# Optimization experiments

Hardware: AMD Instinct MI355X
Metric: run time of the kernel (lower is better)

The kernel has to match this reference:

```python
import jax, jax.numpy as jnp
import numpy as np

B, T, D = 4, 512, 128
HID = 64
INIT = 0.02


def setup_inputs() -> dict:
    key = jax.random.key(0)
    ks = jax.random.split(key, 8)
    h = jax.random.normal(ks[0], (B, T, D), dtype=jnp.float32)
    h_src = jax.random.normal(ks[1], (B, T, D), dtype=jnp.float32)
    # Linear weights stored as (in, out); init std matches cfg.v_phi_init_scale, biases zero.
    W1 = jax.random.normal(ks[2], (3 * D, HID), dtype=jnp.float32) * INIT
    b1 = jnp.zeros((HID,), dtype=jnp.float32)
    W2 = jax.random.normal(ks[3], (HID, HID), dtype=jnp.float32) * INIT
    b2 = jnp.zeros((HID,), dtype=jnp.float32)
    W3 = jax.random.normal(ks[4], (HID, 1), dtype=jnp.float32) * INIT
    b3 = jnp.zeros((1,), dtype=jnp.float32)
    return {"h": h, "h_src": h_src, "W1": W1, "b1": b1, "W2": W2, "b2": b2, "W3": W3, "b3": b3}


def reference(h, h_src, W1, b1, W2, b2, W3, b3):
    # feats = cat(h_q, h_k, h_q - h_k) @ W1  ==  h_q @ (W1q + W1d) + h_k @ (W1k - W1d)
    # This avoids materializing the (B,T,T,3D) concat tensor while computing identical math.
    W1q, W1k, W1d = W1[:D], W1[D:2 * D], W1[2 * D:]
    pq = jnp.einsum('btd,dh->bth', h, W1q + W1d)        # (B,T,HID)
    pk = jnp.einsum('bsd,dh->bsh', h_src, W1k - W1d)    # (B,T,HID)
    x = jax.nn.gelu(pq[:, :, None, :] + pk[:, None, :, :] + b1, approximate=False)  # (B,T,T,HID)
    x = jax.nn.gelu(jnp.einsum('btsh,hk->btsk', x, W2) + b2, approximate=False)
    out = jnp.einsum('btsh,ho->btso', x, W3) + b3       # (B,T,T,1)
    return out[..., 0]                                   # (B,T,T)
```

## Files before the change

kernel.cpp:

```cpp
#include <hip/hip_runtime.h>

#define BB 4
#define TT 512
#define SS 512
#define DD 128
#define HID 64

typedef _Float16 f16;
typedef f16 f16x4 __attribute__((ext_vector_type(4)));
typedef f16 f16x8 __attribute__((ext_vector_type(8)));
typedef float f32x4 __attribute__((ext_vector_type(4)));

#define SPLAT8(c) ((f16x8){(f16)(c),(f16)(c),(f16)(c),(f16)(c),(f16)(c),(f16)(c),(f16)(c),(f16)(c)})

__device__ __forceinline__ f16x8 gelu_pk8(f16x8 x) {
    f16x8 xc = __builtin_elementwise_min(
                   __builtin_elementwise_max(x, SPLAT8(-3.0f)), SPLAT8(3.0f));
    f16x8 xh = xc * SPLAT8(0.5f);
    f16x8 v  = xh * xh;
    f16x8 p  = __builtin_elementwise_fma(v, SPLAT8(-1.96106e-3f), SPLAT8(1.709184e-2f));
    p = __builtin_elementwise_fma(p, v, SPLAT8(-6.617536e-2f));
    p = __builtin_elementwise_fma(p, v, SPLAT8(1.571632e-1f));
    p = __builtin_elementwise_fma(p, v, SPLAT8(-2.665228e-1f));
    p = __builtin_elementwise_fma(p, v, SPLAT8(3.99050e-1f));
    f16x8 t = v * p;
    return __builtin_elementwise_fma(t, SPLAT8(4.0f), x * SPLAT8(0.5f));
}

__global__ __launch_bounds__(256) void pqk_kernel(
    const float* __restrict__ h, const float* __restrict__ h_src,
    const float* __restrict__ W1, const float* __restrict__ b1,
    f16* __restrict__ pq, f16* __restrict__ pk)
{
    const int tid  = threadIdx.x;
    const int wave = tid >> 6;
    const int lane = tid & 63;
    const int g = lane >> 4;
    const int r = lane & 15;

    const int half = blockIdx.x >> 5;
    const int row0 = (blockIdx.x & 31) * 64 + wave * 16;

    const float* src = half ? h_src : h;
    const float* Wa  = W1 + (half ? DD * HID : 0);
    const float* Wd  = W1 + 2 * DD * HID;
    const float  sgn = half ? -1.0f : 1.0f;
    f16* dst = half ? pk : pq;

    f16x8 aw[4][4];
    #pragma unroll
    for (int ks = 0; ks < 4; ++ks) {
        #pragma unroll
        for (int nb = 0; nb < 4; ++nb) {
            const float* wa = Wa + (ks * 32 + g * 8) * HID + nb * 16 + r;
            const float* wd = Wd + (ks * 32 + g * 8) * HID + nb * 16 + r;
            f16x8 v;
            #pragma unroll
            for (int i = 0; i < 8; ++i)
                v[i] = (f16)fmaf(sgn, wd[i * HID], wa[i * HID]);
            aw[ks][nb] = v;
        }
    }

    f16x8 bx[4];
    const float* srow = src + (size_t)(row0 + r) * DD + g * 8;
    #pragma unroll
    for (int ks = 0; ks < 4; ++ks) {
        float4 q0 = *(const float4*)(srow + ks * 32);
        float4 q1 = *(const float4*)(srow + ks * 32 + 4);
        f16x8 v;
        v[0] = (f16)q0.x; v[1] = (f16)q0.y; v[2] = (f16)q0.z; v[3] = (f16)q0.w;
        v[4] = (f16)q1.x; v[5] = (f16)q1.y; v[6] = (f16)q1.z; v[7] = (f16)q1.w;
        bx[ks] = v;
    }

    #pragma unroll
    for (int nb = 0; nb < 4; ++nb) {
        f32x4 acc;
        if (half == 0) {
            float4 bv = *(const float4*)(b1 + nb * 16 + g * 4);
            acc = (f32x4){bv.x, bv.y, bv.z, bv.w};
        } else {
            acc = (f32x4){0.f, 0.f, 0.f, 0.f};
        }
        #pragma unroll
        for (int ks = 0; ks < 4; ++ks)
            acc = __builtin_amdgcn_mfma_f32_16x16x32_f16(aw[ks][nb], bx[ks], acc, 0, 0, 0);
        f16x4 w;
        w[0] = (f16)acc[0]; w[1] = (f16)acc[1];
        w[2] = (f16)acc[2]; w[3] = (f16)acc[3];
        *(f16x4*)(dst + (size_t)(row0 + r) * HID + nb * 16 + g * 4) = w;
    }
}

#define LOADKV(KV0, KV1, CHUNK) {                                         \
    const f16* p_ = pkbase + (size_t)(CHUNK) * 16 * HID;                  \
    (KV0) = *(const f16x8*)(p_);                                          \
    (KV1) = *(const f16x8*)(p_ + 32); }

#define STAGE1(KV0, KV1) {                                                \
    a0 = gelu_pk8(pq0 + (KV0));                                           \
    a1 = gelu_pk8(pq1 + (KV1)); }

#define DOMFMA() {                                                        \
    _Pragma("unroll")                                                     \
    for (int nb = 0; nb < 4; ++nb) {                                      \
        acc[nb] = __builtin_amdgcn_mfma_f32_16x16x32_f16(bw[0][nb], a0, b2i[nb], 0, 0, 0); \
        acc[nb] = __builtin_amdgcn_mfma_f32_16x16x32_f16(bw[1][nb], a1, acc[nb], 0, 0, 0); } }

#define STAGE2(C) {                                                       \
    float tl0 = 0.0f, tl1 = 0.0f, tq0 = 0.0f, tq1 = 0.0f;                 \
    _Pragma("unroll")                                                     \
    for (int nb = 0; nb < 4; ++nb) {                                      \
        _Pragma("unroll")                                                 \
        for (int reg = 0; reg < 4; ++reg) {                               \
            float y = acc[nb][reg];                                       \
            float u = y * y;                                              \
            float cw = (reg == 0) ? w3v[nb].x : (reg == 1) ? w3v[nb].y    \
                     : (reg == 2) ? w3v[nb].z : w3v[nb].w;                \
            if (nb & 1) { tl1 = fmaf(y, cw, tl1); tq1 = fmaf(u, cw, tq1); } \
            else        { tl0 = fmaf(y, cw, tl0); tq0 = fmaf(u, cw, tq0); } \
        }                                                                 \
    }                                                                     \
    float t0 = fmaf(tl0 + tl1, 0.5f, 0.39894228f * (tq0 + tq1));          \
    t0 += __shfl_xor(t0, 16);                                             \
    t0 += __shfl_xor(t0, 32);                                             \
    if (lane < 16) orow[(C) * 16 + lane] = t0 + b3v; }

__global__ __launch_bounds__(256, 4) void main_kernel(
    const f16* __restrict__ pq, const f16* __restrict__ pk,
    const float* __restrict__ W2, const float* __restrict__ b2,
    const float* __restrict__ W3, const float* __restrict__ b3,
    float* __restrict__ out)
{
    const int tid  = threadIdx.x;
    const int wave = tid >> 6;
    const int lane = tid & 63;
    const int g = lane >> 4;
    const int r = lane & 15;

    const int wu  = blockIdx.x * 4 + wave;
    const int bt  = wu >> 2;
    const int sb0 = (wu & 3) * 128;
    const int b   = bt >> 9;

    f16x8 bw[2][4];
    #pragma unroll
    for (int kh = 0; kh < 2; ++kh) {
        #pragma unroll
        for (int nb = 0; nb < 4; ++nb) {
            const float* src = W2 + (kh * 32 + g * 8) * HID + nb * 16 + r;
            f16x8 v;
            #pragma unroll
            for (int i = 0; i < 8; ++i) v[i] = (f16)src[i * HID];
            bw[kh][nb] = v;
        }
    }

    const f16* pqrow = pq + (size_t)bt * HID + g * 8;
    f16x8 pq0 = *(const f16x8*)(pqrow);
    f16x8 pq1 = *(const f16x8*)(pqrow + 32);

    f32x4 b2i[4];
    float4 w3v[4];
    #pragma unroll
    for (int nb = 0; nb < 4; ++nb) {
        float4 bv = *(const float4*)(b2 + nb * 16 + g * 4);
        b2i[nb] = (f32x4){bv.x, bv.y, bv.z, bv.w};
        w3v[nb] = *(const float4*)(W3 + nb * 16 + g * 4);
    }
    const float b3v = b3[0];

    const f16* pkbase = pk + ((size_t)b * SS + sb0 + r) * HID + g * 8;
    float* orow = out + (size_t)bt * SS + sb0;

    f16x8 kvA0, kvA1, kvB0, kvB1;
    f16x8 a0, a1;
    f32x4 acc[4];

    LOADKV(kvA0, kvA1, 0)
    LOADKV(kvB0, kvB1, 1)
    STAGE1(kvA0, kvA1)

    #pragma unroll
    for (int cc = 0; cc < 4; ++cc) {
        DOMFMA()
        if (cc < 3) LOADKV(kvA0, kvA1, 2 * cc + 2)
        STAGE1(kvB0, kvB1)
        STAGE2(2 * cc)

        DOMFMA()
        if (cc < 3) {
            LOADKV(kvB0, kvB1, 2 * cc + 3)
            STAGE1(kvA0, kvA1)
        }
        STAGE2(2 * cc + 1)
    }
}

extern "C" void kernel_launch(void* const* d_in, const int* in_sizes, int n_in,
                              void* d_out, int out_size, void* d_ws, size_t ws_size,
                              hipStream_t stream) {
    const float* h     = (const float*)d_in[0];
    const float* h_src = (const float*)d_in[1];
    const float* W1    = (const float*)d_in[2];
    const float* b1    = (const float*)d_in[3];
    const float* W2    = (const float*)d_in[4];
    const float* b2    = (const float*)d_in[5];
    const float* W3    = (const float*)d_in[6];
    const float* b3    = (const float*)d_in[7];
    float* out = (float*)d_out;

    f16* pq = (f16*)d_ws;
    f16* pk = pq + (size_t)BB * TT * HID;

    pqk_kernel<<<64, 256, 0, stream>>>(h, h_src, W1, b1, pq, pk);
    main_kernel<<<BB * TT * (SS / 128) / 4, 256, 0, stream>>>(pq, pk, W2, b2, W3, b3, out);
}
```

Measured before the change: 36.17 us.

## Fold linear part of second GELU into extra MFMA and absorb b2 algebraically

The second-layer GELU is expanded as a polynomial in the pre-activation. Its linear term, projected through W3, is precomputed as a vector (wlin) plus a constant in an extra block of the first kernel, and the main kernel evaluates it with one additional MFMA pair instead of per-element FMAs. The first GELU is reformulated on the halved input so the 0.5 scaling folds into the pq/pk add and the clamp is removed. This trades a fifth MFMA chain per chunk for fewer VALU ops in the epilogue. The unclamped f16 polynomial and the dropped b2 in the quadratic term may change accuracy, and clvp sits at wlin+HID in f16 units, which is only 4-byte aligned.

Measured after the change: 33.48 us. -7.4%, faster.

```diff
diff --git a/kernel.cpp b/kernel.cpp
--- a/kernel.cpp
+++ b/kernel.cpp
@@ -13,25 +13,43 @@
 
 #define SPLAT8(c) ((f16x8){(f16)(c),(f16)(c),(f16)(c),(f16)(c),(f16)(c),(f16)(c),(f16)(c),(f16)(c)})
 
-__device__ __forceinline__ f16x8 gelu_pk8(f16x8 x) {
-    f16x8 xc = __builtin_elementwise_min(
-                   __builtin_elementwise_max(x, SPLAT8(-3.0f)), SPLAT8(3.0f));
-    f16x8 xh = xc * SPLAT8(0.5f);
-    f16x8 v  = xh * xh;
-    f16x8 p  = __builtin_elementwise_fma(v, SPLAT8(-1.96106e-3f), SPLAT8(1.709184e-2f));
-    p = __builtin_elementwise_fma(p, v, SPLAT8(-6.617536e-2f));
-    p = __builtin_elementwise_fma(p, v, SPLAT8(1.571632e-1f));
-    p = __builtin_elementwise_fma(p, v, SPLAT8(-2.665228e-1f));
-    p = __builtin_elementwise_fma(p, v, SPLAT8(3.99050e-1f));
-    f16x8 t = v * p;
-    return __builtin_elementwise_fma(t, SPLAT8(4.0f), x * SPLAT8(0.5f));
+__device__ __forceinline__ f16x8 gelu_h(f16x8 xh) {
+    f16x8 v = xh * xh;
+    f16x8 p = __builtin_elementwise_fma(v, SPLAT8(-7.84424e-3f), SPLAT8(6.836736e-2f));
+    p = __builtin_elementwise_fma(p, v, SPLAT8(-2.6470144e-1f));
+    p = __builtin_elementwise_fma(p, v, SPLAT8(6.286528e-1f));
+    p = __builtin_elementwise_fma(p, v, SPLAT8(-1.0660912f));
+    p = __builtin_elementwise_fma(p, v, SPLAT8(1.596200f));
+    return __builtin_elementwise_fma(v, p, xh);
 }
 
 __global__ __launch_bounds__(256) void pqk_kernel(
     const float* __restrict__ h, const float* __restrict__ h_src,
     const float* __restrict__ W1, const float* __restrict__ b1,
-    f16* __restrict__ pq, f16* __restrict__ pk)
+    const float* __restrict__ W2, const float* __restrict__ b2,
+    const float* __restrict__ W3, const float* __restrict__ b3,
+    f16* __restrict__ pq, f16* __restrict__ pk,
+    f16* __restrict__ wlin, float* __restrict__ clvp)
 {
+    if (blockIdx.x == 64) {
+        const int t = threadIdx.x;
+        if (t < HID) {
+            float accw = 0.0f;
+            #pragma unroll 8
+            for (int n = 0; n < HID; ++n) {
+                float ln = W3[n] * fmaf(0.79788456f, b2[n], 0.5f);
+                accw = fmaf(W2[t * HID + n], ln, accw);
+            }
+            wlin[t] = (f16)accw;
+        } else if (t == HID) {
+            float cl = b3[0];
+            for (int n = 0; n < HID; ++n)
+                cl = fmaf(W3[n], fmaf(0.39894228f * b2[n], b2[n], 0.5f * b2[n]), cl);
+            clvp[0] = cl;
+        }
+        return;
+    }
+
     const int tid  = threadIdx.x;
     const int wave = tid >> 6;
     const int lane = tid & 63;
@@ -99,17 +117,19 @@
     (KV1) = *(const f16x8*)(p_ + 32); }
 
 #define STAGE1(KV0, KV1) {                                                \
-    a0 = gelu_pk8(pq0 + (KV0));                                           \
-    a1 = gelu_pk8(pq1 + (KV1)); }
+    a0 = gelu_h(__builtin_elementwise_fma((KV0), SPLAT8(0.5f), pqh0));    \
+    a1 = gelu_h(__builtin_elementwise_fma((KV1), SPLAT8(0.5f), pqh1)); }
 
 #define DOMFMA() {                                                        \
     _Pragma("unroll")                                                     \
     for (int nb = 0; nb < 4; ++nb) {                                      \
-        acc[nb] = __builtin_amdgcn_mfma_f32_16x16x32_f16(bw[0][nb], a0, b2i[nb], 0, 0, 0); \
-        acc[nb] = __builtin_amdgcn_mfma_f32_16x16x32_f16(bw[1][nb], a1, acc[nb], 0, 0, 0); } }
+        acc[nb] = __builtin_amdgcn_mfma_f32_16x16x32_f16(bw[0][nb], a0, Z4, 0, 0, 0); \
+        acc[nb] = __builtin_amdgcn_mfma_f32_16x16x32_f16(bw[1][nb], a1, acc[nb], 0, 0, 0); } \
+    accL = __builtin_amdgcn_mfma_f32_16x16x32_f16(wlA0, a0, Z4, 0, 0, 0); \
+    accL = __builtin_amdgcn_mfma_f32_16x16x32_f16(wlA1, a1, accL, 0, 0, 0); }
 
 #define STAGE2(C) {                                                       \
-    float tl0 = 0.0f, tl1 = 0.0f, tq0 = 0.0f, tq1 = 0.0f;                 \
+    float tq0 = 0.0f, tq1 = 0.0f;                                         \
     _Pragma("unroll")                                                     \
     for (int nb = 0; nb < 4; ++nb) {                                      \
         _Pragma("unroll")                                                 \
@@ -118,19 +138,19 @@
             float u = y * y;                                              \
             float cw = (reg == 0) ? w3v[nb].x : (reg == 1) ? w3v[nb].y    \
                      : (reg == 2) ? w3v[nb].z : w3v[nb].w;                \
-            if (nb & 1) { tl1 = fmaf(y, cw, tl1); tq1 = fmaf(u, cw, tq1); } \
-            else        { tl0 = fmaf(y, cw, tl0); tq0 = fmaf(u, cw, tq0); } \
+            if (nb & 1) tq1 = fmaf(u, cw, tq1);                           \
+            else        tq0 = fmaf(u, cw, tq0);                           \
         }                                                                 \
     }                                                                     \
-    float t0 = fmaf(tl0 + tl1, 0.5f, 0.39894228f * (tq0 + tq1));          \
+    float t0 = fmaf(tq0 + tq1, 0.39894228f, 0.25f * accL[0]);             \
     t0 += __shfl_xor(t0, 16);                                             \
     t0 += __shfl_xor(t0, 32);                                             \
-    if (lane < 16) orow[(C) * 16 + lane] = t0 + b3v; }
+    if (lane < 16) orow[(C) * 16 + lane] = t0 + clv; }
 
 __global__ __launch_bounds__(256, 4) void main_kernel(
     const f16* __restrict__ pq, const f16* __restrict__ pk,
-    const float* __restrict__ W2, const float* __restrict__ b2,
-    const float* __restrict__ W3, const float* __restrict__ b3,
+    const float* __restrict__ W2, const float* __restrict__ W3,
+    const f16* __restrict__ wlin, const float* __restrict__ clvp,
     float* __restrict__ out)
 {
     const int tid  = threadIdx.x;
@@ -158,18 +178,18 @@
     }
 
     const f16* pqrow = pq + (size_t)bt * HID + g * 8;
-    f16x8 pq0 = *(const f16x8*)(pqrow);
-    f16x8 pq1 = *(const f16x8*)(pqrow + 32);
-
-    f32x4 b2i[4];
+    f16x8 pqh0 = (*(const f16x8*)(pqrow)) * SPLAT8(0.5f);
+    f16x8 pqh1 = (*(const f16x8*)(pqrow + 32)) * SPLAT8(0.5f);
+
+    f16x8 wlA0 = *(const f16x8*)(wlin + g * 8);
+    f16x8 wlA1 = *(const f16x8*)(wlin + 32 + g * 8);
+
     float4 w3v[4];
     #pragma unroll
-    for (int nb = 0; nb < 4; ++nb) {
-        float4 bv = *(const float4*)(b2 + nb * 16 + g * 4);
-        b2i[nb] = (f32x4){bv.x, bv.y, bv.z, bv.w};
+    for (int nb = 0; nb < 4; ++nb)
         w3v[nb] = *(const float4*)(W3 + nb * 16 + g * 4);
-    }
-    const float b3v = b3[0];
+    const float clv = clvp[0];
+    const f32x4 Z4 = {0.f, 0.f, 0.f, 0.f};
 
     const f16* pkbase = pk + ((size_t)b * SS + sb0 + r) * HID + g * 8;
     float* orow = out + (size_t)bt * SS + sb0;
@@ -177,6 +197,7 @@
     f16x8 kvA0, kvA1, kvB0, kvB1;
     f16x8 a0, a1;
     f32x4 acc[4];
+    f32x4 accL;
 
     LOADKV(kvA0, kvA1, 0)
     LOADKV(kvB0, kvB1, 1)
@@ -211,9 +232,13 @@
     const float* b3    = (const float*)d_in[7];
     float* out = (float*)d_out;
 
-    f16* pq = (f16*)d_ws;
-    f16* pk = pq + (size_t)BB * TT * HID;
-
-    pqk_kernel<<<64, 256, 0, stream>>>(h, h_src, W1, b1, pq, pk);
-    main_kernel<<<BB * TT * (SS / 128) / 4, 256, 0, stream>>>(pq, pk, W2, b2, W3, b3, out);
-}
+    f16* pq   = (f16*)d_ws;
+    f16* pk   = pq + (size_t)BB * TT * HID;
+    f16* wlin = pk + (size_t)BB * SS * HID;
+    float* clvp = (float*)(wlin + HID);
+
+    pqk_kernel<<<65, 256, 0, stream>>>(h, h_src, W1, b1, W2, b2, W3, b3,
+                                       pq, pk, wlin, clvp);
+    main_kernel<<<BB * TT * (SS / 128) / 4, 256, 0, stream>>>(pq, pk, W2, W3,
+                                                              wlin, clvp, out);
+}
```
